# Kernel tuning notes

Measured on AMD Instinct MI355X. Metric: run time of the kernel, lower is better.

Reference implementation:

```python
import jax, jax.numpy as jnp
import numpy as np

B, X, Y, Z, C = 2, 96, 96, 64, 32
K_BG = K_FG = 8
LOG_PROB_SCALE = 200.0


def _make_gmm(key, K, C):
    k1, k2, k3 = jax.random.split(key, 3)
    # mixture weights divided by 2, as in the torch module
    w = jax.nn.softmax(jax.random.normal(k1, (K,))) / 2.0
    mu = jax.random.normal(k2, (K, C), dtype=jnp.float32)
    A = 0.1 * jax.random.normal(k3, (K, C, C), dtype=jnp.float32)
    d = 0.5 + jnp.abs(jnp.diagonal(A, axis1=-2, axis2=-1))  # positive diagonal
    L = jnp.tril(A, -1) + jax.vmap(jnp.diag)(d)             # valid lower Cholesky
    return w.astype(jnp.float32), mu, L


def setup_inputs() -> dict:
    key = jax.random.key(0)
    kf, kb, kg = jax.random.split(key, 3)
    feature_map = jax.random.normal(kf, (B, X, Y, Z, C), dtype=jnp.float32)
    w_bg, mu_bg, L_bg = _make_gmm(kb, K_BG, C)
    w_fg, mu_fg, L_fg = _make_gmm(kg, K_FG, C)
    return {
        "feature_map": feature_map,
        "weights_bg": w_bg, "means_bg": mu_bg, "chol_bg": L_bg,
        "weights_fg": w_fg, "means_fg": mu_fg, "chol_fg": L_fg,
    }


def reference(feature_map, weights_bg, means_bg, chol_bg,
              weights_fg, means_fg, chol_fg):
    Bv, Xv, Yv, Zv, Cv = feature_map.shape
    w = jnp.concatenate([weights_bg, weights_fg])      # [K]
    mu = jnp.concatenate([means_bg, means_fg])         # [K,C]
    L = jnp.concatenate([chol_bg, chol_fg])            # [K,C,C] lower tri

    eye = jnp.eye(Cv, dtype=L.dtype)
    Linv = jax.vmap(lambda l: jax.scipy.linalg.solve_triangular(l, eye, lower=True))(L)
    logdet = jnp.sum(jnp.log(jnp.diagonal(L, axis1=-2, axis2=-1)), axis=-1)  # [K]
    const = -0.5 * Cv * float(np.log(2.0 * np.pi))

    def body(dens, p):
        wk, muk, Lik, ldk = p
        # whitened residual y = L^{-1}(x - mu): [B,X,Y,Z,C]
        y = jnp.einsum('bxyzc,dc->bxyzd', feature_map - muk, Lik)
        logp = const - ldk - 0.5 * jnp.sum(y * y, axis=-1)  # MVN log_prob [B,X,Y,Z]
        return dens + wk * jnp.exp(logp / LOG_PROB_SCALE), None

    dens0 = jnp.zeros(feature_map.shape[:4], dtype=feature_map.dtype)
    dens, _ = jax.lax.scan(body, dens0, (w, mu, Linv, logdet))

    # torch loop runs frac in range(Z-1): last z-slice stays zero
    mask = (jnp.arange(Zv) < Zv - 1).astype(dens.dtype)
    dens = dens * mask  # broadcast over last axis
    return dens[:, None]  # [B,1,X,Y,Z]
```

## Files before the change

kernel.cpp:

```cpp
#include <hip/hip_runtime.h>
#include <hip/hip_bf16.h>
#include <cstring>

#define NVOX (2 * 96 * 96 * 64)
#define K_TOT 16
#define N_TILES (NVOX / 128)

typedef __attribute__((ext_vector_type(8)))  short short8;
typedef __attribute__((ext_vector_type(16))) float f32x16;
typedef __attribute__((ext_vector_type(2)))  float f32x2;
typedef __attribute__((ext_vector_type(2)))  unsigned int uint2v;

#define WS_UF 8192
#define WS_HW 8704
#define WS_FLOATS 8736

__device__ __align__(16) float g_ws[WS_FLOATS];

static __device__ __forceinline__ unsigned short f2b(float f) {
    __hip_bfloat16 h = __float2bfloat16(f);
    unsigned short u;
    __builtin_memcpy(&u, &h, 2);
    return u;
}

static __device__ __forceinline__ int pack2_bf16(float f0, float f1) {
    unsigned a, b;
    __builtin_memcpy(&a, &f0, 4);
    __builtin_memcpy(&b, &f1, 4);
    return (int)__builtin_amdgcn_perm(b + 0x8000u, a + 0x8000u, 0x07060302u);
}

static __device__ __forceinline__ short8 cvt8(float4 lo, float4 hi) {
    int p0 = pack2_bf16(lo.x, lo.y);
    int p1 = pack2_bf16(lo.z, lo.w);
    int p2 = pack2_bf16(hi.x, hi.y);
    int p3 = pack2_bf16(hi.z, hi.w);
    int v[4] = {p0, p1, p2, p3};
    short8 r;
    __builtin_memcpy(&r, v, 16);
    return r;
}

static __device__ __forceinline__ float cross_half_sum(float p) {
#if __has_builtin(__builtin_amdgcn_permlane32_swap)
    unsigned pu;
    __builtin_memcpy(&pu, &p, 4);
    uint2v r = __builtin_amdgcn_permlane32_swap(pu, pu, false, false);
    unsigned a = r.x, b = r.y;
    float fa, fb;
    __builtin_memcpy(&fa, &a, 4);
    __builtin_memcpy(&fb, &b, 4);
    return fa + fb;
#else
    return p + __shfl_xor(p, 32);
#endif
}

__global__ void gmm_prep_kernel(const float* __restrict__ wb, const float* __restrict__ mb,
                                const float* __restrict__ Lb, const float* __restrict__ wf,
                                const float* __restrict__ mf, const float* __restrict__ Lf) {
    int k   = blockIdx.x;
    int tid = threadIdx.x;

    __shared__ float Lsh[1024];
    __shared__ float Lish[1024];
    __shared__ float ush[32];

    const float* L  = (k < 8) ? (Lb + k * 1024) : (Lf + (k - 8) * 1024);
    const float* mu = (k < 8) ? (mb + k * 32)   : (mf + (k - 8) * 32);

    for (int i = tid; i < 1024; i += 64) Lsh[i] = L[i];
    __syncthreads();

    if (tid < 32) {
        int j = tid;
        float col[32];
#pragma unroll
        for (int i = 0; i < 32; ++i) {
            float s = (i == j) ? 1.0f : 0.0f;
#pragma unroll
            for (int m = 0; m < i; ++m) s = fmaf(-Lsh[i * 32 + m], col[m], s);
            float val = s / Lsh[i * 32 + i];
            col[i] = (i >= j) ? val : 0.0f;
        }
#pragma unroll
        for (int i = 0; i < 32; ++i) Lish[i * 32 + j] = col[i];
    }
    __syncthreads();
    if (tid < 32) {
        int d = tid;
        float s = 0.0f;
        for (int c = 0; c <= d; ++c) s = fmaf(Lish[d * 32 + c], mu[c], s);
        ush[d] = s;
    }
    __syncthreads();

    unsigned short* wsA = (unsigned short*)g_ws;
    int m  = tid & 31;
    int kq = tid >> 5;
#pragma unroll
    for (int hf = 0; hf < 2; ++hf) {
        unsigned short* dst = wsA + (size_t)(((k * 2 + hf) * 64 + tid) * 8);
#pragma unroll
        for (int j = 0; j < 8; ++j)
            dst[j] = f2b(Lish[m * 32 + hf * 16 + kq * 8 + j]);
    }
    if (tid < 32) {
        int h = tid >> 4, r = tid & 15;
        g_ws[WS_UF + k * 32 + tid] = -ush[(r & 3) + 8 * (r >> 2) + 4 * h];
    }
    if (tid == 0) {
        float ld = 0.0f;
        for (int i = 0; i < 32; ++i) ld += logf(Lsh[i * 32 + i]);
        const float cconst = -0.5f * 32.0f * 1.8378770664093453f;
        const float log2e  = 1.4426950408889634f;
        g_ws[WS_HW + k * 2]     = (cconst - ld) * (1.0f / 200.0f) * log2e;
        g_ws[WS_HW + k * 2 + 1] = (k < 8) ? wb[k] : wf[k - 8];
    }
}

__global__ __launch_bounds__(256, 3) void gmm_density_kernel(
        const float* __restrict__ fm, float* __restrict__ out) {
    __shared__ __align__(16) float smem[WS_FLOATS];
    {
        const float4* src = (const float4*)g_ws;
        float4* dst = (float4*)smem;
        for (int i = threadIdx.x; i < WS_FLOATS / 4; i += 256) dst[i] = src[i];
    }
    __syncthreads();
    const unsigned short* sWf = (const unsigned short*)smem;
    const float* sUf = smem + WS_UF;
    const float* sHW = smem + WS_HW;

    const int lane = threadIdx.x & 63;
    const int c    = lane & 31;
    const int h    = lane >> 5;
    const int tile = (blockIdx.x * 256 + (int)threadIdx.x) >> 6;
    size_t vbase = (size_t)tile * 128;

    const float SCALE = -0.0036067376022224085f;

    short8 Blo[4], Bhi[4];
#pragma unroll
    for (int g = 0; g < 4; ++g) {
        const float* xb = fm + (vbase + g * 32 + c) * 32 + h * 8;
        float4 a0 = *(const float4*)(xb + 0);
        float4 a1 = *(const float4*)(xb + 4);
        float4 b0 = *(const float4*)(xb + 16);
        float4 b1 = *(const float4*)(xb + 20);
        Blo[g] = cvt8(a0, a1);
        Bhi[g] = cvt8(b0, b1);
    }

    float dens[4] = {0.f, 0.f, 0.f, 0.f};
    for (int kc = 0; kc < K_TOT; ++kc) {
        short8 Alo = *(const short8*)(sWf + ((size_t)(kc * 2 + 0) * 64 + lane) * 8);
        short8 Ahi = *(const short8*)(sWf + ((size_t)(kc * 2 + 1) * 64 + lane) * 8);
        f32x16 Cu = *(const f32x16*)(sUf + kc * 32 + h * 16);
        float h2 = sHW[kc * 2], wk = sHW[kc * 2 + 1];
#pragma unroll
        for (int g = 0; g < 4; ++g) {
            f32x16 d = __builtin_amdgcn_mfma_f32_32x32x16_bf16(Alo, Blo[g], Cu, 0, 0, 0);
            d = __builtin_amdgcn_mfma_f32_32x32x16_bf16(Ahi, Bhi[g], d, 0, 0, 0);
            const f32x2* dp = (const f32x2*)&d;
            f32x2 acc0 = dp[0] * dp[0];
            f32x2 acc1 = dp[1] * dp[1];
#pragma unroll
            for (int r = 1; r < 4; ++r) {
                acc0 += dp[2 * r + 0] * dp[2 * r + 0];
                acc1 += dp[2 * r + 1] * dp[2 * r + 1];
            }
            f32x2 accs = acc0 + acc1;
            float p = accs[0] + accs[1];
            float pt = cross_half_sum(p);
            dens[g] = fmaf(wk, __builtin_amdgcn_exp2f(fmaf(pt, SCALE, h2)), dens[g]);
        }
    }

#pragma unroll
    for (int gg = 0; gg < 2; ++gg) {
        int g = h * 2 + gg;
        float val = dens[g];
        if (c == 31 && (g & 1)) val = 0.f;
        out[vbase + g * 32 + c] = val;
    }
}

extern "C" void kernel_launch(void* const* d_in, const int* in_sizes, int n_in,
                              void* d_out, int out_size, void* d_ws, size_t ws_size,
                              hipStream_t stream) {
    const float* fm = (const float*)d_in[0];
    const float* wb = (const float*)d_in[1];
    const float* mb = (const float*)d_in[2];
    const float* Lb = (const float*)d_in[3];
    const float* wf = (const float*)d_in[4];
    const float* mf = (const float*)d_in[5];
    const float* Lf = (const float*)d_in[6];
    float* out = (float*)d_out;
    (void)d_ws; (void)ws_size;

    gmm_prep_kernel<<<K_TOT, 64, 0, stream>>>(wb, mb, Lb, wf, mf, Lf);
    gmm_density_kernel<<<N_TILES / 4, 256, 0, stream>>>(fm, out);
}
```

Before: 242.4 us.

## Make density kernel persistent with async global-to-LDS prefetch of next tile

Converts the density kernel into a persistent grid of 256 blocks of 7 waves, each wave looping over tiles. The next tile's features are prefetched directly into a per-wave LDS slab via global_load_lds while the current tile's MFMA and exp work runs. This aims to hide global load latency behind compute. The large LDS slabs reduce occupancy to one block per CU and create some tail imbalance across waves.

Result: slower. 255.6 us (+5.5%).

```diff
diff --git a/kernel.cpp b/kernel.cpp
--- a/kernel.cpp
+++ b/kernel.cpp
@@ -5,6 +5,11 @@
 #define NVOX (2 * 96 * 96 * 64)
 #define K_TOT 16
 #define N_TILES (NVOX / 128)
+#define N_BLOCKS 256
+#define WAVES_PB 7
+#define THREADS (WAVES_PB * 64)
+#define N_WAVES_G (N_BLOCKS * WAVES_PB)
+#define SLAB_FLOATS 4096
 
 typedef __attribute__((ext_vector_type(8)))  short short8;
 typedef __attribute__((ext_vector_type(16))) float f32x16;
@@ -57,6 +62,13 @@
 #endif
 }
 
+static __device__ __forceinline__ void gl_lds16(const float* g, float* l) {
+    __builtin_amdgcn_global_load_lds(
+        (const __attribute__((address_space(1))) void*)g,
+        (__attribute__((address_space(3))) void*)l,
+        16, 0, 0);
+}
+
 __global__ void gmm_prep_kernel(const float* __restrict__ wb, const float* __restrict__ mb,
                                 const float* __restrict__ Lb, const float* __restrict__ wf,
                                 const float* __restrict__ mf, const float* __restrict__ Lf) {
@@ -120,13 +132,13 @@
     }
 }
 
-__global__ __launch_bounds__(256, 3) void gmm_density_kernel(
+__global__ __launch_bounds__(THREADS, 2) void gmm_density_kernel(
         const float* __restrict__ fm, float* __restrict__ out) {
-    __shared__ __align__(16) float smem[WS_FLOATS];
+    __shared__ __align__(16) float smem[WS_FLOATS + WAVES_PB * SLAB_FLOATS];
     {
         const float4* src = (const float4*)g_ws;
         float4* dst = (float4*)smem;
-        for (int i = threadIdx.x; i < WS_FLOATS / 4; i += 256) dst[i] = src[i];
+        for (int i = threadIdx.x; i < WS_FLOATS / 4; i += THREADS) dst[i] = src[i];
     }
     __syncthreads();
     const unsigned short* sWf = (const unsigned short*)smem;
@@ -136,55 +148,85 @@
     const int lane = threadIdx.x & 63;
     const int c    = lane & 31;
     const int h    = lane >> 5;
-    const int tile = (blockIdx.x * 256 + (int)threadIdx.x) >> 6;
-    size_t vbase = (size_t)tile * 128;
+    const int wv   = threadIdx.x >> 6;
+    float* slab    = smem + WS_FLOATS + wv * SLAB_FLOATS;
+    const int wid  = blockIdx.x * WAVES_PB + wv;
 
     const float SCALE = -0.0036067376022224085f;
 
+#define ISSUE_TILE(tile) do {                                                 \
+        _Pragma("unroll")                                                     \
+        for (int g_ = 0; g_ < 4; ++g_) {                                      \
+            const float* xb_ = fm + (((size_t)(tile) * 128 + g_ * 32 + c) * 32 + h * 8); \
+            gl_lds16(xb_ + 0,  slab + (g_ * 4 + 0) * 256);                    \
+            gl_lds16(xb_ + 4,  slab + (g_ * 4 + 1) * 256);                    \
+            gl_lds16(xb_ + 16, slab + (g_ * 4 + 2) * 256);                    \
+            gl_lds16(xb_ + 20, slab + (g_ * 4 + 3) * 256);                    \
+        }                                                                     \
+    } while (0)
+
+    int t = wid;
+    ISSUE_TILE(t);
+
     short8 Blo[4], Bhi[4];
-#pragma unroll
-    for (int g = 0; g < 4; ++g) {
-        const float* xb = fm + (vbase + g * 32 + c) * 32 + h * 8;
-        float4 a0 = *(const float4*)(xb + 0);
-        float4 a1 = *(const float4*)(xb + 4);
-        float4 b0 = *(const float4*)(xb + 16);
-        float4 b1 = *(const float4*)(xb + 20);
-        Blo[g] = cvt8(a0, a1);
-        Bhi[g] = cvt8(b0, b1);
-    }
-
-    float dens[4] = {0.f, 0.f, 0.f, 0.f};
-    for (int kc = 0; kc < K_TOT; ++kc) {
-        short8 Alo = *(const short8*)(sWf + ((size_t)(kc * 2 + 0) * 64 + lane) * 8);
-        short8 Ahi = *(const short8*)(sWf + ((size_t)(kc * 2 + 1) * 64 + lane) * 8);
-        f32x16 Cu = *(const f32x16*)(sUf + kc * 32 + h * 16);
-        float h2 = sHW[kc * 2], wk = sHW[kc * 2 + 1];
+    while (true) {
+        const int nt = t + N_WAVES_G;
+        const bool more = (nt < N_TILES);
+
+        asm volatile("s_waitcnt vmcnt(0)" ::: "memory");
+        __builtin_amdgcn_sched_barrier(0);
 #pragma unroll
         for (int g = 0; g < 4; ++g) {
-            f32x16 d = __builtin_amdgcn_mfma_f32_32x32x16_bf16(Alo, Blo[g], Cu, 0, 0, 0);
-            d = __builtin_amdgcn_mfma_f32_32x32x16_bf16(Ahi, Bhi[g], d, 0, 0, 0);
-            const f32x2* dp = (const f32x2*)&d;
-            f32x2 acc0 = dp[0] * dp[0];
-            f32x2 acc1 = dp[1] * dp[1];
-#pragma unroll
-            for (int r = 1; r < 4; ++r) {
-                acc0 += dp[2 * r + 0] * dp[2 * r + 0];
-                acc1 += dp[2 * r + 1] * dp[2 * r + 1];
+            float4 a0 = *(const float4*)(slab + (g * 4 + 0) * 256 + lane * 4);
+            float4 a1 = *(const float4*)(slab + (g * 4 + 1) * 256 + lane * 4);
+            float4 b0 = *(const float4*)(slab + (g * 4 + 2) * 256 + lane * 4);
+            float4 b1 = *(const float4*)(slab + (g * 4 + 3) * 256 + lane * 4);
+            Blo[g] = cvt8(a0, a1);
+            Bhi[g] = cvt8(b0, b1);
+        }
+        asm volatile("s_waitcnt lgkmcnt(0)" ::: "memory");
+        __builtin_amdgcn_sched_barrier(0);
+        if (more) ISSUE_TILE(nt);
+        __builtin_amdgcn_sched_barrier(0);
+
+        float dens[4] = {0.f, 0.f, 0.f, 0.f};
+        for (int kc = 0; kc < K_TOT; ++kc) {
+            short8 Alo = *(const short8*)(sWf + ((size_t)(kc * 2 + 0) * 64 + lane) * 8);
+            short8 Ahi = *(const short8*)(sWf + ((size_t)(kc * 2 + 1) * 64 + lane) * 8);
+            f32x16 Cu = *(const f32x16*)(sUf + kc * 32 + h * 16);
+            float h2 = sHW[kc * 2], wk = sHW[kc * 2 + 1];
+#pragma unroll
+            for (int g = 0; g < 4; ++g) {
+                f32x16 d = __builtin_amdgcn_mfma_f32_32x32x16_bf16(Alo, Blo[g], Cu, 0, 0, 0);
+                d = __builtin_amdgcn_mfma_f32_32x32x16_bf16(Ahi, Bhi[g], d, 0, 0, 0);
+                const f32x2* dp = (const f32x2*)&d;
+                f32x2 acc0 = dp[0] * dp[0];
+                f32x2 acc1 = dp[1] * dp[1];
+#pragma unroll
+                for (int r = 1; r < 4; ++r) {
+                    acc0 += dp[2 * r + 0] * dp[2 * r + 0];
+                    acc1 += dp[2 * r + 1] * dp[2 * r + 1];
+                }
+                f32x2 accs = acc0 + acc1;
+                float p = accs[0] + accs[1];
+                float pt = cross_half_sum(p);
+                dens[g] = fmaf(wk, __builtin_amdgcn_exp2f(fmaf(pt, SCALE, h2)), dens[g]);
             }
-            f32x2 accs = acc0 + acc1;
-            float p = accs[0] + accs[1];
-            float pt = cross_half_sum(p);
-            dens[g] = fmaf(wk, __builtin_amdgcn_exp2f(fmaf(pt, SCALE, h2)), dens[g]);
-        }
-    }
-
-#pragma unroll
-    for (int gg = 0; gg < 2; ++gg) {
-        int g = h * 2 + gg;
-        float val = dens[g];
-        if (c == 31 && (g & 1)) val = 0.f;
-        out[vbase + g * 32 + c] = val;
-    }
+        }
+
+        {
+            size_t vbase = (size_t)t * 128;
+            float v0 = h ? dens[2] : dens[0];
+            float v1 = h ? dens[3] : dens[1];
+            if (c == 31) v1 = 0.f;
+            out[vbase + (size_t)(h * 2 + 0) * 32 + c] = v0;
+            out[vbase + (size_t)(h * 2 + 1) * 32 + c] = v1;
+        }
+
+        if (!more) break;
+        t = nt;
+    }
+#undef ISSUE_TILE
 }
 
 extern "C" void kernel_launch(void* const* d_in, const int* in_sizes, int n_in,
@@ -201,5 +243,5 @@
     (void)d_ws; (void)ws_size;
 
     gmm_prep_kernel<<<K_TOT, 64, 0, stream>>>(wb, mb, Lb, wf, mf, Lf);
-    gmm_density_kernel<<<N_TILES / 4, 256, 0, stream>>>(fm, out);
-}
+    gmm_density_kernel<<<N_BLOCKS, THREADS, 0, stream>>>(fm, out);
+}
```
